# Kernel tuning notes

Hardware: AMD Instinct MI355X
Metric: run time of the kernel (lower is better)

Reference implementation:

```python
import jax, jax.numpy as jnp
import numpy as np

N, E, H, DK, DV = 4096, 1024, 16, 64, 64


def setup_inputs() -> dict:
    key = jax.random.key(0)
    ks = jax.random.split(key, 5)
    x = jax.random.normal(ks[0], (N, E), dtype=jnp.float32)
    # xavier-uniform-like scale for weights
    def xavier(k, shape, fan_in, fan_out):
        lim = (6.0 / (fan_in + fan_out)) ** 0.5
        return jax.random.uniform(k, shape, dtype=jnp.float32, minval=-lim, maxval=lim)
    Wq = xavier(ks[1], (H, E, DK), E, DK)
    Wk = xavier(ks[2], (H, E, DK), E, DK)
    Wv = xavier(ks[3], (H, E, DV), E, DV)
    Wo = xavier(ks[4], (H * DV, E), H * DV, E)
    return {"x": x, "Wq": Wq, "Wk": Wk, "Wv": Wv, "Wo": Wo}


def reference(x, Wq, Wk, Wv, Wo):
    d_key = Wq.shape[-1]
    # per-head projections, batched over heads: [H, N, d]
    q = jnp.einsum('ne,hed->hnd', x, Wq)
    k = jnp.einsum('ne,hed->hnd', x, Wk)
    v = jnp.einsum('ne,hed->hnd', x, Wv)
    scores = jnp.einsum('hnd,hmd->hnm', q, k) / jnp.sqrt(jnp.float32(d_key))
    attn = jax.nn.softmax(scores, axis=-1)  # non-causal full attention
    out = jnp.einsum('hnm,hmd->hnd', attn, v)  # [H, N, DV]
    # concat heads along feature dim: [N, H*DV]
    concatenated = jnp.transpose(out, (1, 0, 2)).reshape(x.shape[0], -1)
    return concatenated @ Wo
```

## Files before the change

kernel.cpp:

```cpp
#include <hip/hip_runtime.h>
#include <hip/hip_bf16.h>


typedef __attribute__((ext_vector_type(8))) short s16x8;
typedef __attribute__((ext_vector_type(4))) float f32x4;
typedef __attribute__((ext_vector_type(16))) float f32x16;

#define MFMA16(A, B, C) __builtin_amdgcn_mfma_f32_16x16x32_bf16((A), (B), (C), 0, 0, 0)
#define MFMA32(A, B, C) __builtin_amdgcn_mfma_f32_32x32x16_bf16((A), (B), (C), 0, 0, 0)

union U8 { s16x8 h; unsigned u[4]; };

__device__ __forceinline__ unsigned short f2bf(float f) {
  unsigned int u = __float_as_uint(f);
  unsigned int r = (u + 0x7FFFu + ((u >> 16) & 1u)) >> 16;
  return (unsigned short)r;
}

__device__ __forceinline__ float expv(float x) {
  float r; asm("v_exp_f32 %0, %1" : "=v"(r) : "v"(x)); return r;
}

__device__ __forceinline__ unsigned cvtpk(float lo, float hi) {
  unsigned d; asm("v_cvt_pk_bf16_f32 %0, %1, %2" : "=v"(d) : "v"(lo), "v"(hi)); return d;
}

__device__ __forceinline__ void pl32swap(unsigned& a, unsigned& b) {
  asm("v_permlane32_swap_b32 %0, %1" : "+v"(a), "+v"(b));
}

__device__ __forceinline__ void gload16(const void* g, void* l) {
  __builtin_amdgcn_global_load_lds(
      (const __attribute__((address_space(1))) unsigned*)g,
      (__attribute__((address_space(3))) unsigned*)l, 16, 0, 0);
}


__global__ __launch_bounds__(256) void convert_x(const float* __restrict__ x,
                                                 unsigned short* __restrict__ xb) {
  unsigned i = blockIdx.x * 256u + threadIdx.x;
  float4 v = reinterpret_cast<const float4*>(x)[i];
  ushort4 o;
  o.x = f2bf(v.x); o.y = f2bf(v.y); o.z = f2bf(v.z); o.w = f2bf(v.w);
  reinterpret_cast<ushort4*>(xb)[i] = o;
}

__global__ __launch_bounds__(256)
void transpose_cast(const float* __restrict__ src, unsigned short* __restrict__ dst,
                    int R, int C) {
  __shared__ float t[64][65];
  const int b = blockIdx.x, rt = blockIdx.y, ct = blockIdx.z;
  const int q = threadIdx.x & 3;
  const float* S = src + ((size_t)b * R + rt * 64) * C + ct * 64;
  {
    const int r = threadIdx.x >> 2;
#pragma unroll
    for (int i = 0; i < 4; ++i) {
      float4 v = *reinterpret_cast<const float4*>(S + (size_t)r * C + (i * 4 + q) * 4);
      t[r][(i * 4 + q) * 4 + 0] = v.x;
      t[r][(i * 4 + q) * 4 + 1] = v.y;
      t[r][(i * 4 + q) * 4 + 2] = v.z;
      t[r][(i * 4 + q) * 4 + 3] = v.w;
    }
  }
  __syncthreads();
  const int c = threadIdx.x >> 2;
  unsigned short* D = dst + ((size_t)b * C + ct * 64 + c) * R + rt * 64;
#pragma unroll
  for (int i = 0; i < 2; ++i) {
    int rb = q * 16 + i * 8;
    union { ushort4 v[2]; unsigned short s[8]; } pk;
#pragma unroll
    for (int k = 0; k < 8; ++k) pk.s[k] = f2bf(t[rb + k][c]);
    *reinterpret_cast<ushort4*>(D + rb) = pk.v[0];
    *reinterpret_cast<ushort4*>(D + rb + 4) = pk.v[1];
  }
}

__global__ __launch_bounds__(512, 4)
void qkv_gemm(const unsigned short* __restrict__ xb,
              const unsigned short* __restrict__ wqt,
              const unsigned short* __restrict__ wkt,
              const unsigned short* __restrict__ wvt,
              unsigned short* __restrict__ Q,
              unsigned short* __restrict__ K,
              unsigned short* __restrict__ Vt) {
  __shared__ char lds[16384 + 24576];
  char* At = lds;
  char* Bl = lds + 16384;

  const int tid = threadIdx.x;
  const int w = tid >> 6, lane = tid & 63;
  const int lr = lane & 15, lg = lane >> 4;
  const int mh = w >> 2, nq = w & 3;
  const int h = blockIdx.y;
  const int m0 = blockIdx.x * 128;

  f32x4 acc[4][3] = {};

  unsigned aoff[4][2], boff[3][2];
#pragma unroll
  for (int m = 0; m < 4; ++m) {
    int row = mh * 64 + m * 16 + lr;
#pragma unroll
    for (int ks = 0; ks < 2; ++ks)
      aoff[m][ks] = (unsigned)((row * 128 + ks * 64 + lg * 16) ^ ((row & 7) << 4));
  }
#pragma unroll
  for (int n = 0; n < 3; ++n) {
    int row = nq * 48 + n * 16 + lr;
#pragma unroll
    for (int ks = 0; ks < 2; ++ks)
      boff[n][ks] = (unsigned)((row * 128 + ks * 64 + lg * 16) ^ ((row & 7) << 4));
  }

  for (int kk = 0; kk < 16; ++kk) {
#pragma unroll
    for (int i = 0; i < 5; ++i) {
      int seg = w * 5 + i;
      if (seg < 16) {
        int row = seg * 8 + (lane >> 3);
        int c = lane & 7;
        gload16(xb + (size_t)(m0 + row) * 1024 + kk * 64 + ((c ^ (row & 7)) * 8),
                At + seg * 1024);
      } else {
        int s2 = seg - 16;
        int row = s2 * 8 + (lane >> 3);
        int mat = row >> 6, mr = row & 63;
        const unsigned short* Wb = (mat == 0 ? wqt : (mat == 1 ? wkt : wvt));
        int c = lane & 7;
        gload16(Wb + h * 65536 + mr * 1024 + kk * 64 + ((c ^ (row & 7)) * 8),
                Bl + s2 * 1024);
      }
    }
    __syncthreads();
#pragma unroll
    for (int ks = 0; ks < 2; ++ks) {
      s16x8 af[4], bf[3];
#pragma unroll
      for (int m = 0; m < 4; ++m) af[m] = *reinterpret_cast<const s16x8*>(At + aoff[m][ks]);
#pragma unroll
      for (int n = 0; n < 3; ++n) bf[n] = *reinterpret_cast<const s16x8*>(Bl + boff[n][ks]);
#pragma unroll
      for (int m = 0; m < 4; ++m)
#pragma unroll
        for (int n = 0; n < 3; ++n)
          acc[m][n] = MFMA16(af[m], bf[n], acc[m][n]);
    }
    __syncthreads();
  }

#pragma unroll
  for (int n = 0; n < 3; ++n) {
    int col = nq * 48 + n * 16 + lr;
    int mat = col >> 6, d = col & 63;
    const float sc = (mat == 0) ? 0.18033688011112042f : 1.0f;
    unsigned short* dst = (mat == 0 ? Q : (mat == 1 ? K : Vt));
#pragma unroll
    for (int m = 0; m < 4; ++m)
#pragma unroll
      for (int r = 0; r < 4; ++r) {
        int row = m0 + mh * 64 + m * 16 + lg * 4 + r;
        unsigned short val = f2bf(acc[m][n][r] * sc);
        if (mat < 2) dst[h * 262144 + row * 64 + d] = val;
        else         dst[h * 262144 + d * 4096 + row] = val;
      }
  }
}

__global__ __launch_bounds__(256)
void attn_kernel(const unsigned short* __restrict__ Q,
                 const unsigned short* __restrict__ K,
                 const unsigned short* __restrict__ Vt,
                 unsigned short* __restrict__ cc) {
  __shared__ char smem[2 * 16384 + 512];
  float* rsf = reinterpret_cast<float*>(smem + 32768);

  const int tid = threadIdx.x;
  const int w = tid >> 6, lane = tid & 63;
  const int l31 = lane & 31, hi = lane >> 5;

  const int lin = blockIdx.x;
  const int cxcd = lin & 7, t = lin >> 3;
  const int h = cxcd * 2 + (t >> 5);
  const int q0 = (t & 31) * 128;

  const unsigned short* Qh = Q + h * 262144;
  const unsigned short* Kh = K + h * 262144;
  const unsigned short* Vh = Vt + h * 262144;

  s16x8 qf[4];
#pragma unroll
  for (int d = 0; d < 4; ++d)
    qf[d] = *reinterpret_cast<const s16x8*>(Qh + (size_t)(q0 + w * 32 + l31) * 64 + d * 16 + hi * 8);

  unsigned koff[8];
#pragma unroll
  for (int k2 = 0; k2 < 2; ++k2)
#pragma unroll
    for (int d = 0; d < 4; ++d) {
      int row = k2 * 32 + l31;
      int ch = (d * 2 + hi) ^ (row & 7);
      koff[k2 * 4 + d] = (unsigned)(row * 128 + ch * 16);
    }
  unsigned voff[8];
#pragma unroll
  for (int n = 0; n < 2; ++n)
#pragma unroll
    for (int ks = 0; ks < 4; ++ks) {
      int row = n * 32 + l31;
      int ch = (ks * 2 + hi) ^ (row & 7);
      voff[n * 4 + ks] = (unsigned)(row * 128 + ch * 16);
    }

  const int so = ((lane & 7) ^ (lane >> 3)) * 8;
  const int rsub = lane >> 3;
  auto stage = [&](int kt, char* buf) {
    char* bK = buf;
    char* bV = buf + 8192;
    const unsigned short* Ksrc = Kh + (size_t)kt * 4096;
    const unsigned short* Vsrc = Vh + kt * 64;
    gload16(Ksrc + (w * 16 + rsub) * 64 + so,                bK + w * 2048);
    gload16(Ksrc + (w * 16 + 8 + rsub) * 64 + so,            bK + w * 2048 + 1024);
    gload16(Vsrc + (size_t)(w * 16 + rsub) * 4096 + so,      bV + w * 2048);
    gload16(Vsrc + (size_t)(w * 16 + 8 + rsub) * 4096 + so,  bV + w * 2048 + 1024);
  };

  f32x16 o0 = {}, o1 = {};
  float rsl = 0.f;

  stage(0, smem);
  __syncthreads();

  for (int kt = 0; kt < 64; ++kt) {
    const int cur = kt & 1;
    char* cb = smem + cur * 16384;
    if (kt < 63) stage(kt + 1, smem + (cur ^ 1) * 16384);

    const char* bK = cb;
    const char* bV = cb + 8192;

    f32x16 s0 = {}, s1 = {};
#pragma unroll
    for (int d = 0; d < 4; ++d) {
      s16x8 a0 = *reinterpret_cast<const s16x8*>(bK + koff[d]);
      s16x8 a1 = *reinterpret_cast<const s16x8*>(bK + koff[4 + d]);
      s0 = MFMA32(a0, qf[d], s0);
      s1 = MFMA32(a1, qf[d], s1);
    }

    s16x8 pa[4];
    {
      float p[16];
#pragma unroll
      for (int r = 0; r < 16; ++r) { p[r] = expv(s0[r]); rsl += p[r]; }
      unsigned a0 = cvtpk(p[0], p[1]), b0 = cvtpk(p[2], p[3]);
      unsigned a1 = cvtpk(p[4], p[5]), b1 = cvtpk(p[6], p[7]);
      pl32swap(a0, a1); pl32swap(b0, b1);
      U8 f; f.u[0] = a0; f.u[1] = b0; f.u[2] = a1; f.u[3] = b1;
      pa[0] = f.h;
      a0 = cvtpk(p[8], p[9]);  b0 = cvtpk(p[10], p[11]);
      a1 = cvtpk(p[12], p[13]); b1 = cvtpk(p[14], p[15]);
      pl32swap(a0, a1); pl32swap(b0, b1);
      U8 g; g.u[0] = a0; g.u[1] = b0; g.u[2] = a1; g.u[3] = b1;
      pa[1] = g.h;
    }
    {
      float p[16];
#pragma unroll
      for (int r = 0; r < 16; ++r) { p[r] = expv(s1[r]); rsl += p[r]; }
      unsigned a0 = cvtpk(p[0], p[1]), b0 = cvtpk(p[2], p[3]);
      unsigned a1 = cvtpk(p[4], p[5]), b1 = cvtpk(p[6], p[7]);
      pl32swap(a0, a1); pl32swap(b0, b1);
      U8 f; f.u[0] = a0; f.u[1] = b0; f.u[2] = a1; f.u[3] = b1;
      pa[2] = f.h;
      a0 = cvtpk(p[8], p[9]);  b0 = cvtpk(p[10], p[11]);
      a1 = cvtpk(p[12], p[13]); b1 = cvtpk(p[14], p[15]);
      pl32swap(a0, a1); pl32swap(b0, b1);
      U8 g; g.u[0] = a0; g.u[1] = b0; g.u[2] = a1; g.u[3] = b1;
      pa[3] = g.h;
    }

#pragma unroll
    for (int ks = 0; ks < 4; ++ks) {
      s16x8 v0 = *reinterpret_cast<const s16x8*>(bV + voff[ks]);
      s16x8 v1 = *reinterpret_cast<const s16x8*>(bV + voff[4 + ks]);
      o0 = MFMA32(pa[ks], v0, o0);
      o1 = MFMA32(pa[ks], v1, o1);
    }

    __syncthreads();
  }

  float rst = rsl + __shfl_xor(rsl, 32, 64);
  float inv;
  asm("v_rcp_f32 %0, %1" : "=v"(inv) : "v"(rst));
  if (lane < 32) rsf[w * 32 + l31] = inv;
  __syncthreads();

#pragma unroll
  for (int reg = 0; reg < 16; ++reg) {
    int qr = (reg & 3) + 8 * (reg >> 2) + 4 * hi;
    float iv = rsf[w * 32 + qr];
    size_t base = (size_t)(q0 + w * 32 + qr) * 1024 + h * 64 + l31;
    cc[base]      = f2bf(o0[reg] * iv);
    cc[base + 32] = f2bf(o1[reg] * iv);
  }
}

__global__ __launch_bounds__(512, 4)
void out_gemm(const unsigned short* __restrict__ A,
              const unsigned short* __restrict__ Bt,
              float* __restrict__ out) {
  __shared__ char lds[16384 + 16384];
  char* At = lds;
  char* Bl = lds + 16384;

  const int tid = threadIdx.x;
  const int w = tid >> 6, lane = tid & 63;
  const int lr = lane & 15, lg = lane >> 4;
  const int mh = w >> 2, nq = w & 3;
  const int m0 = blockIdx.x * 128;
  const int n0 = blockIdx.y * 128;

  f32x4 acc[4][2] = {};

  unsigned aoff[4][2], boff[2][2];
#pragma unroll
  for (int m = 0; m < 4; ++m) {
    int row = mh * 64 + m * 16 + lr;
#pragma unroll
    for (int ks = 0; ks < 2; ++ks)
      aoff[m][ks] = (unsigned)((row * 128 + ks * 64 + lg * 16) ^ ((row & 7) << 4));
  }
#pragma unroll
  for (int n = 0; n < 2; ++n) {
    int row = nq * 32 + n * 16 + lr;
#pragma unroll
    for (int ks = 0; ks < 2; ++ks)
      boff[n][ks] = (unsigned)((row * 128 + ks * 64 + lg * 16) ^ ((row & 7) << 4));
  }

  for (int kk = 0; kk < 16; ++kk) {
#pragma unroll
    for (int i = 0; i < 4; ++i) {
      int seg = w * 4 + i;
      int row = (seg & 15) * 8 + (lane >> 3);
      int c = lane & 7;
      if (seg < 16)
        gload16(A + (size_t)(m0 + row) * 1024 + kk * 64 + ((c ^ (row & 7)) * 8),
                At + seg * 1024);
      else
        gload16(Bt + (size_t)(n0 + row) * 1024 + kk * 64 + ((c ^ (row & 7)) * 8),
                Bl + (seg - 16) * 1024);
    }
    __syncthreads();
#pragma unroll
    for (int ks = 0; ks < 2; ++ks) {
      s16x8 af[4], bf[2];
#pragma unroll
      for (int m = 0; m < 4; ++m) af[m] = *reinterpret_cast<const s16x8*>(At + aoff[m][ks]);
#pragma unroll
      for (int n = 0; n < 2; ++n) bf[n] = *reinterpret_cast<const s16x8*>(Bl + boff[n][ks]);
#pragma unroll
      for (int m = 0; m < 4; ++m)
#pragma unroll
        for (int n = 0; n < 2; ++n)
          acc[m][n] = MFMA16(af[m], bf[n], acc[m][n]);
    }
    __syncthreads();
  }

#pragma unroll
  for (int m = 0; m < 4; ++m)
#pragma unroll
    for (int n = 0; n < 2; ++n)
#pragma unroll
      for (int r = 0; r < 4; ++r) {
        int row = m0 + mh * 64 + m * 16 + lg * 4 + r;
        int col = n0 + nq * 32 + n * 16 + lr;
        out[(size_t)row * 1024 + col] = acc[m][n][r];
      }
}


extern "C" void kernel_launch(void* const* d_in, const int* in_sizes, int n_in,
                              void* d_out, int out_size, void* d_ws, size_t ws_size,
                              hipStream_t stream) {
  const float* x  = (const float*)d_in[0];
  const float* Wq = (const float*)d_in[1];
  const float* Wk = (const float*)d_in[2];
  const float* Wv = (const float*)d_in[3];
  const float* Wo = (const float*)d_in[4];
  float* out = (float*)d_out;
  char* ws = (char*)d_ws;

  unsigned short* xb  = (unsigned short*)(ws);
  unsigned short* wqt = (unsigned short*)(ws + 8388608);
  unsigned short* wkt = (unsigned short*)(ws + 10485760);
  unsigned short* wvt = (unsigned short*)(ws + 12582912);
  unsigned short* wot = (unsigned short*)(ws + 14680064);
  unsigned short* Qb  = (unsigned short*)(ws + 16777216);
  unsigned short* Kb  = (unsigned short*)(ws + 25165824);
  unsigned short* Vtb = (unsigned short*)(ws + 33554432);
  unsigned short* cc  = (unsigned short*)(ws + 41943040);

  convert_x<<<4096, 256, 0, stream>>>(x, xb);
  transpose_cast<<<dim3(16, 16, 1), 256, 0, stream>>>(Wq, wqt, 1024, 64);
  transpose_cast<<<dim3(16, 16, 1), 256, 0, stream>>>(Wk, wkt, 1024, 64);
  transpose_cast<<<dim3(16, 16, 1), 256, 0, stream>>>(Wv, wvt, 1024, 64);
  transpose_cast<<<dim3(1, 16, 16), 256, 0, stream>>>(Wo, wot, 1024, 1024);

  qkv_gemm<<<dim3(32, 16), 512, 0, stream>>>(xb, wqt, wkt, wvt, Qb, Kb, Vtb);
  attn_kernel<<<512, 256, 0, stream>>>(Qb, Kb, Vtb, cc);
  out_gemm<<<dim3(32, 8), 512, 0, stream>>>(cc, wot, out);
}
```

Before: 231.0 us.

## Process 64 query rows per wave in attention to double K/V tile reuse

Each wave in the attention kernel now computes two 32-row query blocks against each staged K/V tile, halving the block count to 256. This doubles reuse of K/V shared-memory tiles and the global loads feeding them, and adds independent MFMA chains per wave. The cost is more accumulator registers and fewer resident waves per CU, which can reduce latency hiding.

```diff
diff --git a/kernel.cpp b/kernel.cpp
--- a/kernel.cpp
+++ b/kernel.cpp
@@ -168,12 +168,28 @@
   }
 }
 
+#define SOFTPACK(S, PA, RS) do {                                            \
+    float p_[16];                                                           \
+    _Pragma("unroll")                                                       \
+    for (int r_ = 0; r_ < 16; ++r_) { p_[r_] = expv((S)[r_]); RS += p_[r_]; } \
+    unsigned a0_ = cvtpk(p_[0], p_[1]), b0_ = cvtpk(p_[2], p_[3]);          \
+    unsigned a1_ = cvtpk(p_[4], p_[5]), b1_ = cvtpk(p_[6], p_[7]);          \
+    pl32swap(a0_, a1_); pl32swap(b0_, b1_);                                 \
+    U8 f_; f_.u[0] = a0_; f_.u[1] = b0_; f_.u[2] = a1_; f_.u[3] = b1_;      \
+    (PA)[0] = f_.h;                                                         \
+    a0_ = cvtpk(p_[8], p_[9]);  b0_ = cvtpk(p_[10], p_[11]);                \
+    a1_ = cvtpk(p_[12], p_[13]); b1_ = cvtpk(p_[14], p_[15]);               \
+    pl32swap(a0_, a1_); pl32swap(b0_, b1_);                                 \
+    U8 g_; g_.u[0] = a0_; g_.u[1] = b0_; g_.u[2] = a1_; g_.u[3] = b1_;      \
+    (PA)[1] = g_.h;                                                         \
+  } while (0)
+
 __global__ __launch_bounds__(256)
 void attn_kernel(const unsigned short* __restrict__ Q,
                  const unsigned short* __restrict__ K,
                  const unsigned short* __restrict__ Vt,
                  unsigned short* __restrict__ cc) {
-  __shared__ char smem[2 * 16384 + 512];
+  __shared__ char smem[2 * 16384 + 1024];
   float* rsf = reinterpret_cast<float*>(smem + 32768);
 
   const int tid = threadIdx.x;
@@ -182,17 +198,19 @@
 
   const int lin = blockIdx.x;
   const int cxcd = lin & 7, t = lin >> 3;
-  const int h = cxcd * 2 + (t >> 5);
-  const int q0 = (t & 31) * 128;
+  const int h = cxcd * 2 + (t >> 4);
+  const int q0 = (t & 15) * 256;
 
   const unsigned short* Qh = Q + h * 262144;
   const unsigned short* Kh = K + h * 262144;
   const unsigned short* Vh = Vt + h * 262144;
 
-  s16x8 qf[4];
-#pragma unroll
-  for (int d = 0; d < 4; ++d)
-    qf[d] = *reinterpret_cast<const s16x8*>(Qh + (size_t)(q0 + w * 32 + l31) * 64 + d * 16 + hi * 8);
+  s16x8 qfA[4], qfB[4];
+#pragma unroll
+  for (int d = 0; d < 4; ++d) {
+    qfA[d] = *reinterpret_cast<const s16x8*>(Qh + (size_t)(q0 + w * 64 + l31) * 64 + d * 16 + hi * 8);
+    qfB[d] = *reinterpret_cast<const s16x8*>(Qh + (size_t)(q0 + w * 64 + 32 + l31) * 64 + d * 16 + hi * 8);
+  }
 
   unsigned koff[8];
 #pragma unroll
@@ -226,8 +244,8 @@
     gload16(Vsrc + (size_t)(w * 16 + 8 + rsub) * 4096 + so,  bV + w * 2048 + 1024);
   };
 
-  f32x16 o0 = {}, o1 = {};
-  float rsl = 0.f;
+  f32x16 oA0 = {}, oA1 = {}, oB0 = {}, oB1 = {};
+  float rsA = 0.f, rsB = 0.f;
 
   stage(0, smem);
   __syncthreads();
@@ -240,71 +258,58 @@
     const char* bK = cb;
     const char* bV = cb + 8192;
 
-    f32x16 s0 = {}, s1 = {};
+    f32x16 sA0 = {}, sA1 = {}, sB0 = {}, sB1 = {};
 #pragma unroll
     for (int d = 0; d < 4; ++d) {
       s16x8 a0 = *reinterpret_cast<const s16x8*>(bK + koff[d]);
       s16x8 a1 = *reinterpret_cast<const s16x8*>(bK + koff[4 + d]);
-      s0 = MFMA32(a0, qf[d], s0);
-      s1 = MFMA32(a1, qf[d], s1);
-    }
-
-    s16x8 pa[4];
-    {
-      float p[16];
-#pragma unroll
-      for (int r = 0; r < 16; ++r) { p[r] = expv(s0[r]); rsl += p[r]; }
-      unsigned a0 = cvtpk(p[0], p[1]), b0 = cvtpk(p[2], p[3]);
-      unsigned a1 = cvtpk(p[4], p[5]), b1 = cvtpk(p[6], p[7]);
-      pl32swap(a0, a1); pl32swap(b0, b1);
-      U8 f; f.u[0] = a0; f.u[1] = b0; f.u[2] = a1; f.u[3] = b1;
-      pa[0] = f.h;
-      a0 = cvtpk(p[8], p[9]);  b0 = cvtpk(p[10], p[11]);
-      a1 = cvtpk(p[12], p[13]); b1 = cvtpk(p[14], p[15]);
-      pl32swap(a0, a1); pl32swap(b0, b1);
-      U8 g; g.u[0] = a0; g.u[1] = b0; g.u[2] = a1; g.u[3] = b1;
-      pa[1] = g.h;
-    }
-    {
-      float p[16];
-#pragma unroll
-      for (int r = 0; r < 16; ++r) { p[r] = expv(s1[r]); rsl += p[r]; }
-      unsigned a0 = cvtpk(p[0], p[1]), b0 = cvtpk(p[2], p[3]);
-      unsigned a1 = cvtpk(p[4], p[5]), b1 = cvtpk(p[6], p[7]);
-      pl32swap(a0, a1); pl32swap(b0, b1);
-      U8 f; f.u[0] = a0; f.u[1] = b0; f.u[2] = a1; f.u[3] = b1;
-      pa[2] = f.h;
-      a0 = cvtpk(p[8], p[9]);  b0 = cvtpk(p[10], p[11]);
-      a1 = cvtpk(p[12], p[13]); b1 = cvtpk(p[14], p[15]);
-      pl32swap(a0, a1); pl32swap(b0, b1);
-      U8 g; g.u[0] = a0; g.u[1] = b0; g.u[2] = a1; g.u[3] = b1;
-      pa[3] = g.h;
-    }
+      sA0 = MFMA32(a0, qfA[d], sA0);
+      sA1 = MFMA32(a1, qfA[d], sA1);
+      sB0 = MFMA32(a0, qfB[d], sB0);
+      sB1 = MFMA32(a1, qfB[d], sB1);
+    }
+
+    s16x8 paA[4], paB[4];
+    SOFTPACK(sA0, paA, rsA);
+    SOFTPACK(sA1, paA + 2, rsA);
+    SOFTPACK(sB0, paB, rsB);
+    SOFTPACK(sB1, paB + 2, rsB);
 
 #pragma unroll
     for (int ks = 0; ks < 4; ++ks) {
       s16x8 v0 = *reinterpret_cast<const s16x8*>(bV + voff[ks]);
       s16x8 v1 = *reinterpret_cast<const s16x8*>(bV + voff[4 + ks]);
-      o0 = MFMA32(pa[ks], v0, o0);
-      o1 = MFMA32(pa[ks], v1, o1);
+      oA0 = MFMA32(paA[ks], v0, oA0);
+      oA1 = MFMA32(paA[ks], v1, oA1);
+      oB0 = MFMA32(paB[ks], v0, oB0);
+      oB1 = MFMA32(paB[ks], v1, oB1);
     }
 
     __syncthreads();
   }
 
-  float rst = rsl + __shfl_xor(rsl, 32, 64);
-  float inv;
-  asm("v_rcp_f32 %0, %1" : "=v"(inv) : "v"(rst));
-  if (lane < 32) rsf[w * 32 + l31] = inv;
+  float rstA = rsA + __shfl_xor(rsA, 32, 64);
+  float rstB = rsB + __shfl_xor(rsB, 32, 64);
+  float invA, invB;
+  asm("v_rcp_f32 %0, %1" : "=v"(invA) : "v"(rstA));
+  asm("v_rcp_f32 %0, %1" : "=v"(invB) : "v"(rstB));
+  if (lane < 32) {
+    rsf[w * 64 + l31] = invA;
+    rsf[w * 64 + 32 + l31] = invB;
+  }
   __syncthreads();
 
 #pragma unroll
   for (int reg = 0; reg < 16; ++reg) {
     int qr = (reg & 3) + 8 * (reg >> 2) + 4 * hi;
-    float iv = rsf[w * 32 + qr];
-    size_t base = (size_t)(q0 + w * 32 + qr) * 1024 + h * 64 + l31;
-    cc[base]      = f2bf(o0[reg] * iv);
-    cc[base + 32] = f2bf(o1[reg] * iv);
+    float ivA = rsf[w * 64 + qr];
+    float ivB = rsf[w * 64 + 32 + qr];
+    size_t bA = (size_t)(q0 + w * 64 + qr) * 1024 + h * 64 + l31;
+    size_t bB = (size_t)(q0 + w * 64 + 32 + qr) * 1024 + h * 64 + l31;
+    cc[bA]      = f2bf(oA0[reg] * ivA);
+    cc[bA + 32] = f2bf(oA1[reg] * ivA);
+    cc[bB]      = f2bf(oB0[reg] * ivB);
+    cc[bB + 32] = f2bf(oB1[reg] * ivB);
   }
 }
 
@@ -412,6 +417,6 @@
   transpose_cast<<<dim3(1, 16, 16), 256, 0, stream>>>(Wo, wot, 1024, 1024);
 
   qkv_gemm<<<dim3(32, 16), 512, 0, stream>>>(xb, wqt, wkt, wvt, Qb, Kb, Vtb);
-  attn_kernel<<<512, 256, 0, stream>>>(Qb, Kb, Vtb, cc);
+  attn_kernel<<<256, 256, 0, stream>>>(Qb, Kb, Vtb, cc);
   out_gemm<<<dim3(32, 8), 512, 0, stream>>>(cc, wot, out);
 }
```

Result: no change. 228.4 us (-1.1%).
